# Kernel optimization log

Measured on AMD Instinct MI355X. Metric: run time of the kernel, lower is better.

Reference implementation:

```python
import jax, jax.numpy as jnp
import numpy as np

VEC_SIZE = 256
N_VECS = 8
N_CHOICES = 2048
BATCH = 2048
EPS = 1e-6
NAND_BIAS = 3.0


def setup_inputs() -> dict:
    key = jax.random.key(0)
    k1, k2 = jax.random.split(key)
    query = jax.random.normal(k1, (BATCH, N_VECS * VEC_SIZE), dtype=jnp.float32)
    weight = jax.random.normal(k2, (N_CHOICES, VEC_SIZE * N_VECS), dtype=jnp.float32)
    # init code overwrites the randn nand_weight with ones + nand_bias
    nand_weight = jnp.full((N_CHOICES, N_VECS), 1.0 + NAND_BIAS, dtype=jnp.float32)
    return {"query": query, "weight": weight, "nand_weight": nand_weight}


def reference(query, weight, nand_weight):
    # [B, n_vecs, vec_size] and [C, n_vecs, vec_size]
    q = query.reshape(-1, N_VECS, VEC_SIZE)
    w = weight.reshape(-1, N_VECS, VEC_SIZE)
    # torch.cosine_similarity clamps each norm to eps
    qn = q / jnp.maximum(jnp.linalg.norm(q, axis=-1, keepdims=True), EPS)
    wn = w / jnp.maximum(jnp.linalg.norm(w, axis=-1, keepdims=True), EPS)
    # broadcast cosine sim expressed as batched matmul: [B, C, n_vecs]
    cos_sim = jnp.einsum('bnd,cnd->bcn', qn, wn)
    cos_sim = jax.nn.leaky_relu(cos_sim)  # slope 0.01, matches F.leaky_relu default
    nw = jax.nn.sigmoid(nand_weight)[None]  # [1, C, n_vecs]
    interpolated = nw * cos_sim + (1.0 - nw) * (1.0 - cos_sim)
    return jnp.prod(interpolated, axis=2)  # [B, C]
```

## Files before the change

kernel.cpp:

```cpp
#include <hip/hip_runtime.h>
#include <math.h>
#include <stdint.h>

#define BATCH    2048
#define NCHOICES 2048
#define NV       8
#define VS       256
#define KTOT     (NV * VS)

typedef unsigned short u16;
typedef __attribute__((ext_vector_type(8))) short    bf16x8;
typedef __attribute__((ext_vector_type(8))) u16      u16x8;
typedef __attribute__((ext_vector_type(4))) float    f32x4;

__device__ __forceinline__ u16 f2bf_rne(float x) {
    unsigned u = __float_as_uint(x);
    return (u16)((u + 0x7FFFu + ((u >> 16) & 1u)) >> 16);
}

__global__ __launch_bounds__(256) void prep_convert(
    const float* __restrict__ Q, const float* __restrict__ W,
    const float* __restrict__ NWT,
    u16* __restrict__ Qh, u16* __restrict__ Ql,
    u16* __restrict__ Wh, u16* __restrict__ Wl,
    float* __restrict__ rq, float* __restrict__ rw, float* __restrict__ snw)
{
    const int row = blockIdx.x;
    const int t   = threadIdx.x;
    const int n   = t >> 5;
    const int l   = t & 31;

    const float* src; u16 *dh, *dl; float* dst;
    if (row < BATCH) {
        src = Q + (size_t)row * KTOT;
        dh = Qh + (size_t)row * KTOT; dl = Ql + (size_t)row * KTOT;
        dst = rq + (size_t)row * NV;
    } else {
        src = W + (size_t)(row - BATCH) * KTOT;
        dh = Wh + (size_t)(row - BATCH) * KTOT; dl = Wl + (size_t)(row - BATCH) * KTOT;
        dst = rw + (size_t)(row - BATCH) * NV;
    }

    const int idx = n * VS + l * 8;
    float4 x0 = *(const float4*)(src + idx);
    float4 x1 = *(const float4*)(src + idx + 4);
    float xs[8] = {x0.x, x0.y, x0.z, x0.w, x1.x, x1.y, x1.z, x1.w};

    u16x8 hv, lv;
    float s = 0.0f;
    #pragma unroll
    for (int j = 0; j < 8; ++j) {
        u16 h = f2bf_rne(xs[j]);
        float hf = __uint_as_float(((unsigned)h) << 16);
        hv[j] = h;
        lv[j] = f2bf_rne(xs[j] - hf);
        s = fmaf(xs[j], xs[j], s);
    }
    *(u16x8*)(dh + idx) = hv;
    *(u16x8*)(dl + idx) = lv;

    #pragma unroll
    for (int m = 1; m < 32; m <<= 1) s += __shfl_xor(s, m, 64);
    if (l == 0) dst[n] = 1.0f / fmaxf(sqrtf(s), 1e-6f);

    if (row >= BATCH && t < NV) {
        const int c = row - BATCH;
        float x = NWT[(size_t)c * NV + t];
        snw[(size_t)c * NV + t] = 1.0f / (1.0f + expf(-x));
    }
}

__device__ __forceinline__ void gload16(const void* g, void* l) {
    __builtin_amdgcn_global_load_lds(
        (__attribute__((address_space(1))) void*)(uintptr_t)g,
        (__attribute__((address_space(3))) void*)(uint32_t)(uintptr_t)l,
        16, 0, 0);
}

#define SWZ(R, G) ((R) * 32 + ((((G) ^ (((R) >> 1) & 3))) << 3))

__global__ __launch_bounds__(256, 2) void nand_mfma(
    const u16* __restrict__ Qh, const u16* __restrict__ Ql,
    const u16* __restrict__ Wh, const u16* __restrict__ Wl,
    const float* __restrict__ rq, const float* __restrict__ rw,
    const float* __restrict__ snw, float* __restrict__ part)
{
    __shared__ __align__(16) u16 L[2][4][128 * 32];

    const int tid  = threadIdx.x;
    const int lane = tid & 63;
    const int wave = tid >> 6;
    const int wr   = (wave >> 1) * 64;
    const int wc   = (wave & 1) * 64;
    const int bm0  = blockIdx.y * 128;
    const int bn0  = blockIdx.x * 128;
    const int z    = blockIdx.z;

    const int fr = lane & 15;
    const int gi = lane >> 4;
    const int ri = (lane >> 4) * 4;

    const int r0 = tid >> 2;
    const int kswz = 8 * ((tid & 3) ^ ((r0 >> 1) & 3));

    const u16* baseA_h = Qh + (size_t)bm0 * KTOT;
    const u16* baseA_l = Ql + (size_t)bm0 * KTOT;
    const u16* baseB_h = Wh + (size_t)bn0 * KTOT;
    const u16* baseB_l = Wl + (size_t)bn0 * KTOT;

    #define STAGE(BUF, KT) do {                                              \
        const int _k0 = z * 512 + (KT) * 32 + kswz;                          \
        const size_t _o0 = (size_t)r0 * KTOT + _k0;                          \
        const size_t _o1 = (size_t)(r0 + 64) * KTOT + _k0;                   \
        u16* _d0 = &L[BUF][0][(tid >> 6) * 512];                             \
        u16* _d1 = &L[BUF][0][((tid >> 6) + 4) * 512];                       \
        gload16(baseA_h + _o0, _d0);        gload16(baseA_h + _o1, _d1);     \
        gload16(baseA_l + _o0, _d0 + 4096); gload16(baseA_l + _o1, _d1 + 4096); \
        gload16(baseB_h + _o0, _d0 + 8192); gload16(baseB_h + _o1, _d1 + 8192); \
        gload16(baseB_l + _o0, _d0 + 12288); gload16(baseB_l + _o1, _d1 + 12288); \
    } while (0)

    f32x4 prod[4][4];
    #pragma unroll
    for (int m = 0; m < 4; ++m)
        #pragma unroll
        for (int n = 0; n < 4; ++n) prod[m][n] = (f32x4){1.f, 1.f, 1.f, 1.f};

    STAGE(0, 0);

    for (int c = 0; c < 2; ++c) {
        const int chunk = z * 2 + c;

        f32x4 acc[4][4];
        #pragma unroll
        for (int m = 0; m < 4; ++m)
            #pragma unroll
            for (int n = 0; n < 4; ++n) acc[m][n] = (f32x4){0.f, 0.f, 0.f, 0.f};

        #pragma unroll 2
        for (int k8 = 0; k8 < 8; ++k8) {
            const int kt  = c * 8 + k8;
            const int buf = kt & 1;
            __syncthreads();
            if (kt < 15) STAGE(buf ^ 1, kt + 1);

            bf16x8 ah[4], al[4], bh[4], bl[4];
            #pragma unroll
            for (int m = 0; m < 4; ++m) {
                ah[m] = *(const bf16x8*)&L[buf][0][SWZ(wr + m * 16 + fr, gi)];
                al[m] = *(const bf16x8*)&L[buf][1][SWZ(wr + m * 16 + fr, gi)];
            }
            #pragma unroll
            for (int n = 0; n < 4; ++n) {
                bh[n] = *(const bf16x8*)&L[buf][2][SWZ(wc + n * 16 + fr, gi)];
                bl[n] = *(const bf16x8*)&L[buf][3][SWZ(wc + n * 16 + fr, gi)];
            }
            #pragma unroll
            for (int m = 0; m < 4; ++m)
                #pragma unroll
                for (int n = 0; n < 4; ++n) {
                    acc[m][n] = __builtin_amdgcn_mfma_f32_16x16x32_bf16(
                        ah[m], bh[n], acc[m][n], 0, 0, 0);
                    acc[m][n] = __builtin_amdgcn_mfma_f32_16x16x32_bf16(
                        ah[m], bl[n], acc[m][n], 0, 0, 0);
                    acc[m][n] = __builtin_amdgcn_mfma_f32_16x16x32_bf16(
                        al[m], bh[n], acc[m][n], 0, 0, 0);
                }
        }

        float rwv[4], vv[4], uu[4];
        #pragma unroll
        for (int n = 0; n < 4; ++n) {
            const int col = bn0 + wc + n * 16 + fr;
            rwv[n] = rw[(size_t)col * NV + chunk];
            float s = snw[(size_t)col * NV + chunk];
            vv[n] = 2.0f * s - 1.0f;
            uu[n] = 1.0f - s;
        }
        #pragma unroll
        for (int m = 0; m < 4; ++m) {
            #pragma unroll
            for (int i = 0; i < 4; ++i) {
                const int row = bm0 + wr + m * 16 + ri + i;
                const float rqv = rq[(size_t)row * NV + chunk];
                #pragma unroll
                for (int n = 0; n < 4; ++n) {
                    float cosv = acc[m][n][i] * rqv * rwv[n];
                    float Lk = fmaxf(cosv, 0.01f * cosv);
                    prod[m][n][i] *= fmaf(Lk, vv[n], uu[n]);
                }
            }
        }
    }

    float* P = part + (size_t)z * BATCH * NCHOICES;
    #pragma unroll
    for (int m = 0; m < 4; ++m)
        #pragma unroll
        for (int i = 0; i < 4; ++i) {
            const int row = bm0 + wr + m * 16 + ri + i;
            float* pr = P + (size_t)row * NCHOICES + bn0 + wc + fr;
            #pragma unroll
            for (int n = 0; n < 4; ++n) pr[n * 16] = prod[m][n][i];
        }
    #undef STAGE
}

__global__ __launch_bounds__(256) void combine_kernel(
    const float* __restrict__ p, float* __restrict__ out)
{
    const size_t NN = (size_t)BATCH * NCHOICES;
    size_t i = ((size_t)blockIdx.x * 256 + threadIdx.x) * 4;
    float4 a = *(const float4*)(p + i);
    float4 b = *(const float4*)(p + NN + i);
    float4 c = *(const float4*)(p + 2 * NN + i);
    float4 d = *(const float4*)(p + 3 * NN + i);
    float4 o;
    o.x = a.x * b.x * c.x * d.x;
    o.y = a.y * b.y * c.y * d.y;
    o.z = a.z * b.z * c.z * d.z;
    o.w = a.w * b.w * c.w * d.w;
    *(float4*)(out + i) = o;
}

__global__ __launch_bounds__(256) void prep_kernel(
    const float* __restrict__ Q, const float* __restrict__ W,
    const float* __restrict__ NWT,
    float* __restrict__ rq, float* __restrict__ rw, float* __restrict__ snw)
{
    const int row = blockIdx.x;
    const int t   = threadIdx.x;
    const int n   = t >> 5;
    const int l   = t & 31;

    const float* src; float* dst;
    if (row < BATCH) { src = Q + (size_t)row * KTOT; dst = rq + (size_t)row * NV; }
    else { src = W + (size_t)(row - BATCH) * KTOT; dst = rw + (size_t)(row - BATCH) * NV; }

    const float* v = src + n * VS + l * 8;
    float4 a = *(const float4*)(v);
    float4 b = *(const float4*)(v + 4);
    float s = a.x*a.x + a.y*a.y + a.z*a.z + a.w*a.w
            + b.x*b.x + b.y*b.y + b.z*b.z + b.w*b.w;
    #pragma unroll
    for (int m = 1; m < 32; m <<= 1) s += __shfl_xor(s, m, 64);
    if (l == 0) dst[n] = 1.0f / fmaxf(sqrtf(s), 1e-6f);
    if (row >= BATCH && t < NV) {
        const int c = row - BATCH;
        float x = NWT[(size_t)c * NV + t];
        snw[(size_t)c * NV + t] = 1.0f / (1.0f + expf(-x));
    }
}

__global__ __launch_bounds__(256, 2) void nand_gemm(
    const float* __restrict__ Q, const float* __restrict__ W,
    const float* __restrict__ rq, const float* __restrict__ rw,
    const float* __restrict__ snw, float* __restrict__ out)
{
    __shared__ __align__(16) float As[16][128 + 4];
    __shared__ __align__(16) float Bs[16][128 + 4];
    __shared__ __align__(16) float rqs[128];
    __shared__ __align__(16) float rws[128];
    __shared__ __align__(16) float sns[128];

    const int tid = threadIdx.x;
    const int tx  = tid & 15;
    const int ty  = tid >> 4;
    const int bm0 = blockIdx.y * 128;
    const int bn0 = blockIdx.x * 128;
    const int lr  = tid >> 2;
    const int lk  = (tid & 3) * 4;

    float prod[8][8];
    #pragma unroll
    for (int i = 0; i < 8; ++i)
        #pragma unroll
        for (int j = 0; j < 8; ++j) prod[i][j] = 1.0f;

    for (int n = 0; n < NV; ++n) {
        float acc[8][8];
        #pragma unroll
        for (int i = 0; i < 8; ++i)
            #pragma unroll
            for (int j = 0; j < 8; ++j) acc[i][j] = 0.0f;

        #pragma unroll 1
        for (int kt = 0; kt < VS / 16; ++kt) {
            const int k0 = n * VS + kt * 16;
            __syncthreads();
            {
                const float* qrow = Q + (size_t)(bm0 + lr) * KTOT + k0 + lk;
                float4 a0 = *(const float4*)(qrow);
                float4 a1 = *(const float4*)(qrow + (size_t)64 * KTOT);
                As[lk + 0][lr] = a0.x; As[lk + 1][lr] = a0.y;
                As[lk + 2][lr] = a0.z; As[lk + 3][lr] = a0.w;
                As[lk + 0][64 + lr] = a1.x; As[lk + 1][64 + lr] = a1.y;
                As[lk + 2][64 + lr] = a1.z; As[lk + 3][64 + lr] = a1.w;

                const float* wrow = W + (size_t)(bn0 + lr) * KTOT + k0 + lk;
                float4 b0 = *(const float4*)(wrow);
                float4 b1 = *(const float4*)(wrow + (size_t)64 * KTOT);
                Bs[lk + 0][lr] = b0.x; Bs[lk + 1][lr] = b0.y;
                Bs[lk + 2][lr] = b0.z; Bs[lk + 3][lr] = b0.w;
                Bs[lk + 0][64 + lr] = b1.x; Bs[lk + 1][64 + lr] = b1.y;
                Bs[lk + 2][64 + lr] = b1.z; Bs[lk + 3][64 + lr] = b1.w;
            }
            if (kt == 0) {
                for (int i = tid; i < 3 * 128; i += 256) {
                    if (i < 128)      rqs[i]       = rq[(size_t)(bm0 + i) * NV + n];
                    else if (i < 256) rws[i - 128] = rw[(size_t)(bn0 + i - 128) * NV + n];
                    else              sns[i - 256] = snw[(size_t)(bn0 + i - 256) * NV + n];
                }
            }
            __syncthreads();

            #pragma unroll
            for (int kk = 0; kk < 16; ++kk) {
                float4 a0 = *(const float4*)&As[kk][ty * 4];
                float4 a1 = *(const float4*)&As[kk][64 + ty * 4];
                float4 b0 = *(const float4*)&Bs[kk][tx * 4];
                float4 b1 = *(const float4*)&Bs[kk][64 + tx * 4];
                float ar[8] = {a0.x, a0.y, a0.z, a0.w, a1.x, a1.y, a1.z, a1.w};
                float br[8] = {b0.x, b0.y, b0.z, b0.w, b1.x, b1.y, b1.z, b1.w};
                #pragma unroll
                for (int i = 0; i < 8; ++i)
                    #pragma unroll
                    for (int j = 0; j < 8; ++j)
                        acc[i][j] = fmaf(ar[i], br[j], acc[i][j]);
            }
        }

        float rwv[8], uu[8], vv[8];
        #pragma unroll
        for (int j = 0; j < 8; ++j) {
            int cc = (j < 4) ? (tx * 4 + j) : (64 + tx * 4 + (j - 4));
            rwv[j] = rws[cc];
            float s = sns[cc];
            uu[j] = 1.0f - s;
            vv[j] = 2.0f * s - 1.0f;
        }
        #pragma unroll
        for (int i = 0; i < 8; ++i) {
            int r = (i < 4) ? (ty * 4 + i) : (64 + ty * 4 + (i - 4));
            float rqv = rqs[r];
            #pragma unroll
            for (int j = 0; j < 8; ++j) {
                float cosv = acc[i][j] * rqv * rwv[j];
                float Lk = fmaxf(cosv, 0.01f * cosv);
                prod[i][j] *= fmaf(Lk, vv[j], uu[j]);
            }
        }
    }

    #pragma unroll
    for (int i = 0; i < 8; ++i) {
        int r = (i < 4) ? (ty * 4 + i) : (64 + ty * 4 + (i - 4));
        float* orow = out + (size_t)(bm0 + r) * NCHOICES + bn0;
        float4 o0 = {prod[i][0], prod[i][1], prod[i][2], prod[i][3]};
        float4 o1 = {prod[i][4], prod[i][5], prod[i][6], prod[i][7]};
        *(float4*)(orow + tx * 4)      = o0;
        *(float4*)(orow + 64 + tx * 4) = o1;
    }
}

extern "C" void kernel_launch(void* const* d_in, const int* in_sizes, int n_in,
                              void* d_out, int out_size, void* d_ws, size_t ws_size,
                              hipStream_t stream)
{
    const float* Q   = (const float*)d_in[0];
    const float* W   = (const float*)d_in[1];
    const float* NWT = (const float*)d_in[2];
    float* out = (float*)d_out;

    char* w = (char*)d_ws;
    float* rq  = (float*)w; w += (size_t)BATCH    * NV * 4;
    float* rwn = (float*)w; w += (size_t)NCHOICES * NV * 4;
    float* snw = (float*)w; w += (size_t)NCHOICES * NV * 4;
    u16* Qh = (u16*)w; w += (size_t)BATCH * KTOT * 2;
    u16* Ql = (u16*)w; w += (size_t)BATCH * KTOT * 2;
    u16* Wh = (u16*)w; w += (size_t)NCHOICES * KTOT * 2;
    u16* Wl = (u16*)w; w += (size_t)NCHOICES * KTOT * 2;
    float* part = (float*)w; w += (size_t)4 * BATCH * NCHOICES * 4;
    const size_t needed = (size_t)(w - (char*)d_ws);

    if (ws_size >= needed) {
        prep_convert<<<BATCH + NCHOICES, 256, 0, stream>>>(
            Q, W, NWT, Qh, Ql, Wh, Wl, rq, rwn, snw);
        dim3 grid(NCHOICES / 128, BATCH / 128, 4);
        nand_mfma<<<grid, 256, 0, stream>>>(Qh, Ql, Wh, Wl, rq, rwn, snw, part);
        combine_kernel<<<(BATCH * NCHOICES / 4) / 256, 256, 0, stream>>>(part, out);
    } else {
        prep_kernel<<<BATCH + NCHOICES, 256, 0, stream>>>(Q, W, NWT, rq, rwn, snw);
        dim3 grid(NCHOICES / 128, BATCH / 128);
        nand_gemm<<<grid, 256, 0, stream>>>(Q, W, rq, rwn, snw, out);
    }
}
```

Before: 91.04 us.

## Restructure split-bf16 MFMA GEMM into 8-wave 128x256 tiles with triple-buffered interleaved pipeline

Replaces the 4-wave 128x128 MFMA kernel with an 8-wave 128x256 tile that uses a three-stage LDS ring. Global-to-LDS prefetches are split into A, B-high and B-low pieces, each interleaved with a quarter of the MFMA work, with explicit barriers, s_setprio and vmcnt waits. The K split drops from 4 to 2, which halves the partial-product buffer and the combine kernel's reads. The goal is to hide memory latency and raise MFMA utilisation. In exchange the grid has fewer blocks (256), LDS use is larger, and the hand-placed waitcnt/barrier scheme is fragile.

```diff
diff --git a/kernel.cpp b/kernel.cpp
--- a/kernel.cpp
+++ b/kernel.cpp
@@ -6,7 +6,7 @@
 #define NCHOICES 2048
 #define NV       8
 #define VS       256
-#define KTOT     (NV * VS)
+#define KTOT     2048
 
 typedef unsigned short u16;
 typedef __attribute__((ext_vector_type(8))) short    bf16x8;
@@ -79,46 +79,64 @@
 
 #define SWZ(R, G) ((R) * 32 + ((((G) ^ (((R) >> 1) & 3))) << 3))
 
-__global__ __launch_bounds__(256, 2) void nand_mfma(
+#define BARRIER() do { asm volatile("" ::: "memory"); \
+                       __builtin_amdgcn_s_barrier();  \
+                       asm volatile("" ::: "memory"); } while (0)
+
+__global__ __launch_bounds__(512, 2) void nand_mfma8(
     const u16* __restrict__ Qh, const u16* __restrict__ Ql,
     const u16* __restrict__ Wh, const u16* __restrict__ Wl,
     const float* __restrict__ rq, const float* __restrict__ rw,
     const float* __restrict__ snw, float* __restrict__ part)
 {
-    __shared__ __align__(16) u16 L[2][4][128 * 32];
+    __shared__ __align__(16) u16 L[3][24576];
 
     const int tid  = threadIdx.x;
     const int lane = tid & 63;
     const int wave = tid >> 6;
-    const int wr   = (wave >> 1) * 64;
-    const int wc   = (wave & 1) * 64;
+    const int wr   = (wave >> 2) * 64;
+    const int wc   = (wave & 3) * 64;
     const int bm0  = blockIdx.y * 128;
-    const int bn0  = blockIdx.x * 128;
+    const int bn0  = blockIdx.x * 256;
     const int z    = blockIdx.z;
+    const int kb   = z * 1024;
 
     const int fr = lane & 15;
     const int gi = lane >> 4;
-    const int ri = (lane >> 4) * 4;
-
-    const int r0 = tid >> 2;
-    const int kswz = 8 * ((tid & 3) ^ ((r0 >> 1) & 3));
-
-    const u16* baseA_h = Qh + (size_t)bm0 * KTOT;
-    const u16* baseA_l = Ql + (size_t)bm0 * KTOT;
-    const u16* baseB_h = Wh + (size_t)bn0 * KTOT;
-    const u16* baseB_l = Wl + (size_t)bn0 * KTOT;
-
-    #define STAGE(BUF, KT) do {                                              \
-        const int _k0 = z * 512 + (KT) * 32 + kswz;                          \
-        const size_t _o0 = (size_t)r0 * KTOT + _k0;                          \
-        const size_t _o1 = (size_t)(r0 + 64) * KTOT + _k0;                   \
-        u16* _d0 = &L[BUF][0][(tid >> 6) * 512];                             \
-        u16* _d1 = &L[BUF][0][((tid >> 6) + 4) * 512];                       \
-        gload16(baseA_h + _o0, _d0);        gload16(baseA_h + _o1, _d1);     \
-        gload16(baseA_l + _o0, _d0 + 4096); gload16(baseA_l + _o1, _d1 + 4096); \
-        gload16(baseB_h + _o0, _d0 + 8192); gload16(baseB_h + _o1, _d1 + 8192); \
-        gload16(baseB_l + _o0, _d0 + 12288); gload16(baseB_l + _o1, _d1 + 12288); \
-    } while (0)
+    const int ri = gi * 4;
+
+    const int gr  = tid >> 2;
+    const int gg  = tid & 3;
+    const int gsw = (gg ^ ((gr >> 1) & 3)) * 8;
+
+    const u16* sAh  = Qh + (size_t)(bm0 + gr) * KTOT + kb + gsw;
+    const u16* sAl  = Ql + (size_t)(bm0 + gr) * KTOT + kb + gsw;
+    const u16* sB0h = Wh + (size_t)(bn0 + gr) * KTOT + kb + gsw;
+    const u16* sB1h = Wh + (size_t)(bn0 + 128 + gr) * KTOT + kb + gsw;
+    const u16* sB0l = Wl + (size_t)(bn0 + gr) * KTOT + kb + gsw;
+    const u16* sB1l = Wl + (size_t)(bn0 + 128 + gr) * KTOT + kb + gsw;
+
+    #define STAGE_A(B, T)  do { u16* Lb_ = &L[B][0];                        \
+        gload16(sAh  + (T) * 32, Lb_ + tid * 8);                            \
+        gload16(sAl  + (T) * 32, Lb_ + 4096  + tid * 8); } while (0)
+    #define STAGE_BH(B, T) do { u16* Lb_ = &L[B][0];                        \
+        gload16(sB0h + (T) * 32, Lb_ + 8192  + tid * 8);                    \
+        gload16(sB1h + (T) * 32, Lb_ + 12288 + tid * 8); } while (0)
+    #define STAGE_BL(B, T) do { u16* Lb_ = &L[B][0];                        \
+        gload16(sB0l + (T) * 32, Lb_ + 16384 + tid * 8);                    \
+        gload16(sB1l + (T) * 32, Lb_ + 20480 + tid * 8); } while (0)
+
+    #define RD_A(M) do {                                                    \
+        ah[M] = *(const bf16x8*)(Lb + SWZ(wr + (M) * 16 + fr, gi));         \
+        al[M] = *(const bf16x8*)(Lb + 4096 + SWZ(wr + (M) * 16 + fr, gi)); } while (0)
+    #define RD_B(N) do {                                                    \
+        bh[N] = *(const bf16x8*)(Lb + 8192  + SWZ(wc + (N) * 16 + fr, gi)); \
+        bl[N] = *(const bf16x8*)(Lb + 16384 + SWZ(wc + (N) * 16 + fr, gi)); } while (0)
+
+    #define MM(M, N) do {                                                   \
+        acc[M][N] = __builtin_amdgcn_mfma_f32_16x16x32_bf16(ah[M], bh[N], acc[M][N], 0, 0, 0); \
+        acc[M][N] = __builtin_amdgcn_mfma_f32_16x16x32_bf16(ah[M], bl[N], acc[M][N], 0, 0, 0); \
+        acc[M][N] = __builtin_amdgcn_mfma_f32_16x16x32_bf16(al[M], bh[N], acc[M][N], 0, 0, 0); } while (0)
 
     f32x4 prod[4][4];
     #pragma unroll
@@ -126,48 +144,23 @@
         #pragma unroll
         for (int n = 0; n < 4; ++n) prod[m][n] = (f32x4){1.f, 1.f, 1.f, 1.f};
 
-    STAGE(0, 0);
-
-    for (int c = 0; c < 2; ++c) {
-        const int chunk = z * 2 + c;
-
-        f32x4 acc[4][4];
+    STAGE_A(0, 0); STAGE_BH(0, 0); STAGE_BL(0, 0);
+    STAGE_A(1, 1); STAGE_BH(1, 1); STAGE_BL(1, 1);
+    asm volatile("s_waitcnt vmcnt(6)" ::: "memory");
+    BARRIER();
+
+    int buf = 0, bufp = 2;
+
+    #pragma unroll 1
+    for (int cc = 0; cc < 4; ++cc) {
+        const int chunk = z * 4 + cc;
+
+        float rqv[4][4];
         #pragma unroll
         for (int m = 0; m < 4; ++m)
             #pragma unroll
-            for (int n = 0; n < 4; ++n) acc[m][n] = (f32x4){0.f, 0.f, 0.f, 0.f};
-
-        #pragma unroll 2
-        for (int k8 = 0; k8 < 8; ++k8) {
-            const int kt  = c * 8 + k8;
-            const int buf = kt & 1;
-            __syncthreads();
-            if (kt < 15) STAGE(buf ^ 1, kt + 1);
-
-            bf16x8 ah[4], al[4], bh[4], bl[4];
-            #pragma unroll
-            for (int m = 0; m < 4; ++m) {
-                ah[m] = *(const bf16x8*)&L[buf][0][SWZ(wr + m * 16 + fr, gi)];
-                al[m] = *(const bf16x8*)&L[buf][1][SWZ(wr + m * 16 + fr, gi)];
-            }
-            #pragma unroll
-            for (int n = 0; n < 4; ++n) {
-                bh[n] = *(const bf16x8*)&L[buf][2][SWZ(wc + n * 16 + fr, gi)];
-                bl[n] = *(const bf16x8*)&L[buf][3][SWZ(wc + n * 16 + fr, gi)];
-            }
-            #pragma unroll
-            for (int m = 0; m < 4; ++m)
-                #pragma unroll
-                for (int n = 0; n < 4; ++n) {
-                    acc[m][n] = __builtin_amdgcn_mfma_f32_16x16x32_bf16(
-                        ah[m], bh[n], acc[m][n], 0, 0, 0);
-                    acc[m][n] = __builtin_amdgcn_mfma_f32_16x16x32_bf16(
-                        ah[m], bl[n], acc[m][n], 0, 0, 0);
-                    acc[m][n] = __builtin_amdgcn_mfma_f32_16x16x32_bf16(
-                        al[m], bh[n], acc[m][n], 0, 0, 0);
-                }
-        }
-
+            for (int i = 0; i < 4; ++i)
+                rqv[m][i] = rq[(size_t)(bm0 + wr + m * 16 + ri + i) * NV + chunk];
         float rwv[4], vv[4], uu[4];
         #pragma unroll
         for (int n = 0; n < 4; ++n) {
@@ -177,20 +170,70 @@
             vv[n] = 2.0f * s - 1.0f;
             uu[n] = 1.0f - s;
         }
-        #pragma unroll
-        for (int m = 0; m < 4; ++m) {
-            #pragma unroll
-            for (int i = 0; i < 4; ++i) {
-                const int row = bm0 + wr + m * 16 + ri + i;
-                const float rqv = rq[(size_t)row * NV + chunk];
+
+        f32x4 acc[4][4];
+        #pragma unroll
+        for (int m = 0; m < 4; ++m)
+            #pragma unroll
+            for (int n = 0; n < 4; ++n) acc[m][n] = (f32x4){0.f, 0.f, 0.f, 0.f};
+
+        #pragma unroll 1
+        for (int t8 = 0; t8 < 8; ++t8) {
+            const int t = cc * 8 + t8;
+            const u16* Lb = &L[buf][0];
+            const bool pf = (t + 2) < 32;
+
+            bf16x8 ah[4], al[4], bh[4], bl[4];
+
+            RD_A(0); RD_A(1); RD_B(0); RD_B(1);
+            if (pf) STAGE_A(bufp, t + 2);
+            BARRIER();
+            __builtin_amdgcn_s_setprio(1);
+            MM(0, 0); MM(0, 1); MM(1, 0); MM(1, 1);
+            __builtin_amdgcn_s_setprio(0);
+            BARRIER();
+
+            RD_B(2); RD_B(3);
+            if (pf) STAGE_BH(bufp, t + 2);
+            BARRIER();
+            __builtin_amdgcn_s_setprio(1);
+            MM(0, 2); MM(0, 3); MM(1, 2); MM(1, 3);
+            __builtin_amdgcn_s_setprio(0);
+            BARRIER();
+
+            RD_A(2); RD_A(3);
+            if (pf) STAGE_BL(bufp, t + 2);
+            BARRIER();
+            __builtin_amdgcn_s_setprio(1);
+            MM(2, 2); MM(2, 3); MM(3, 2); MM(3, 3);
+            __builtin_amdgcn_s_setprio(0);
+            BARRIER();
+
+            __builtin_amdgcn_s_setprio(1);
+            MM(2, 0); MM(2, 1); MM(3, 0); MM(3, 1);
+            __builtin_amdgcn_s_setprio(0);
+
+            if (t < 30) {
+                asm volatile("s_waitcnt vmcnt(6)" ::: "memory");
+                BARRIER();
+            } else if (t == 30) {
+                asm volatile("s_waitcnt vmcnt(0)" ::: "memory");
+                BARRIER();
+            }
+            buf  = (buf  == 2) ? 0 : buf  + 1;
+            bufp = (bufp == 2) ? 0 : bufp + 1;
+        }
+
+        #pragma unroll
+        for (int m = 0; m < 4; ++m)
+            #pragma unroll
+            for (int i = 0; i < 4; ++i)
                 #pragma unroll
                 for (int n = 0; n < 4; ++n) {
-                    float cosv = acc[m][n][i] * rqv * rwv[n];
+                    float cosv = acc[m][n][i] * rqv[m][i] * rwv[n];
                     float Lk = fmaxf(cosv, 0.01f * cosv);
                     prod[m][n][i] *= fmaf(Lk, vv[n], uu[n]);
                 }
-            }
-        }
     }
 
     float* P = part + (size_t)z * BATCH * NCHOICES;
@@ -203,7 +246,13 @@
             #pragma unroll
             for (int n = 0; n < 4; ++n) pr[n * 16] = prod[m][n][i];
         }
-    #undef STAGE
+
+    #undef STAGE_A
+    #undef STAGE_BH
+    #undef STAGE_BL
+    #undef RD_A
+    #undef RD_B
+    #undef MM
 }
 
 __global__ __launch_bounds__(256) void combine_kernel(
@@ -213,13 +262,11 @@
     size_t i = ((size_t)blockIdx.x * 256 + threadIdx.x) * 4;
     float4 a = *(const float4*)(p + i);
     float4 b = *(const float4*)(p + NN + i);
-    float4 c = *(const float4*)(p + 2 * NN + i);
-    float4 d = *(const float4*)(p + 3 * NN + i);
     float4 o;
-    o.x = a.x * b.x * c.x * d.x;
-    o.y = a.y * b.y * c.y * d.y;
-    o.z = a.z * b.z * c.z * d.z;
-    o.w = a.w * b.w * c.w * d.w;
+    o.x = a.x * b.x;
+    o.y = a.y * b.y;
+    o.z = a.z * b.z;
+    o.w = a.w * b.w;
     *(float4*)(out + i) = o;
 }
 
@@ -380,14 +427,14 @@
     u16* Ql = (u16*)w; w += (size_t)BATCH * KTOT * 2;
     u16* Wh = (u16*)w; w += (size_t)NCHOICES * KTOT * 2;
     u16* Wl = (u16*)w; w += (size_t)NCHOICES * KTOT * 2;
-    float* part = (float*)w; w += (size_t)4 * BATCH * NCHOICES * 4;
+    float* part = (float*)w; w += (size_t)2 * BATCH * NCHOICES * 4;
     const size_t needed = (size_t)(w - (char*)d_ws);
 
     if (ws_size >= needed) {
         prep_convert<<<BATCH + NCHOICES, 256, 0, stream>>>(
             Q, W, NWT, Qh, Ql, Wh, Wl, rq, rwn, snw);
-        dim3 grid(NCHOICES / 128, BATCH / 128, 4);
-        nand_mfma<<<grid, 256, 0, stream>>>(Qh, Ql, Wh, Wl, rq, rwn, snw, part);
+        dim3 grid(NCHOICES / 256, BATCH / 128, 2);
+        nand_mfma8<<<grid, 512, 0, stream>>>(Qh, Ql, Wh, Wl, rq, rwn, snw, part);
         combine_kernel<<<(BATCH * NCHOICES / 4) / 256, 256, 0, stream>>>(part, out);
     } else {
         prep_kernel<<<BATCH + NCHOICES, 256, 0, stream>>>(Q, W, NWT, rq, rwn, snw);
```

Result: faster. 83.56 us (-8.2%).
